# Kernel tuning notes

Hardware: AMD Instinct MI355X
Metric: run time of the kernel (lower is better)

Reference implementation:

```python
import jax, jax.numpy as jnp
import numpy as np
import math

N_HEADS = 16
HEAD_DIM = 128  # dim=2048 / 16


def _rope(t, cos, sin):
    # t: [B, S, H, hd]; cos/sin: [1, S, hd//2]
    B, S, H, hd = t.shape
    tr = t.reshape(B, S, H, hd // 2, 2)
    te, to = tr[..., 0], tr[..., 1]
    c = cos[:, :, None, :]
    s = sin[:, :, None, :]
    oe = te * c - to * s
    oo = te * s + to * c
    return jnp.stack([oe, oo], axis=-1).reshape(B, S, H, hd)


def setup_inputs() -> dict:
    key = jax.random.key(0)
    ks = jax.random.split(key, 5)
    B, S, D = 2, 2048, 2048
    hd = HEAD_DIM
    scale = 1.0 / math.sqrt(D)
    x = jax.random.normal(ks[0], (B, S, D), dtype=jnp.float32)
    wq = jax.random.normal(ks[1], (D, D), dtype=jnp.float32) * scale
    wk = jax.random.normal(ks[2], (D, D), dtype=jnp.float32) * scale
    wv = jax.random.normal(ks[3], (D, D), dtype=jnp.float32) * scale
    wo = jax.random.normal(ks[4], (D, D), dtype=jnp.float32) * scale
    # true RoPE angles: freqs = base^(-2i/hd), angles = pos * freqs
    base = 10000.0
    inv_freq = 1.0 / (base ** (np.arange(0, hd, 2, dtype=np.float32) / hd))  # [hd//2]
    pos = np.arange(S, dtype=np.float32)
    ang = pos[:, None] * inv_freq[None, :]  # [S, hd//2]
    pos_cos = jnp.asarray(np.cos(ang))[None]  # [1, S, hd//2]
    pos_sin = jnp.asarray(np.sin(ang))[None]
    return {"x": x, "wq": wq, "wk": wk, "wv": wv, "wo": wo,
            "pos_cos": pos_cos, "pos_sin": pos_sin}


def reference(x, wq, wk, wv, wo, pos_cos, pos_sin):
    B, S, D = x.shape
    H, hd = N_HEADS, HEAD_DIM
    # nn.Linear: y = x @ W.T
    q = (x @ wq.T).reshape(B, S, H, hd)
    k = (x @ wk.T).reshape(B, S, H, hd)
    v = (x @ wv.T).reshape(B, S, H, hd)
    q = _rope(q, pos_cos, pos_sin)
    k = _rope(k, pos_cos, pos_sin)
    # naive full attention, softmax in fp32 (as original)
    scores = jnp.einsum('bqhd,bkhd->bhqk', q, k) / math.sqrt(hd)
    probs = jax.nn.softmax(scores.astype(jnp.float32), axis=-1).astype(q.dtype)
    out = jnp.einsum('bhqk,bkhd->bqhd', probs, v).reshape(B, S, H * hd)
    return out @ wo.T
```

## Files before the change

### kernel.cpp

```cpp
#include <hip/hip_runtime.h>
#include <hip/hip_bf16.h>

typedef __attribute__((ext_vector_type(8))) short short8;
typedef __attribute__((ext_vector_type(4))) float f32x4;
typedef __attribute__((ext_vector_type(16))) float f32x16;
typedef __attribute__((ext_vector_type(8))) unsigned short ushort8v;
typedef __attribute__((ext_vector_type(4))) unsigned int u32x4;

#define AS_GLOBAL __attribute__((address_space(1)))
#define AS_LDS    __attribute__((address_space(3)))

__device__ __forceinline__ void async_ld16(const void* src, void* lds) {
  __builtin_amdgcn_global_load_lds((const AS_GLOBAL unsigned int*)src,
                                   (AS_LDS unsigned int*)lds, 16, 0, 0);
}

__device__ __forceinline__ unsigned short f2bf(float f) {
  unsigned int u = __float_as_uint(f);
  u = (u + 0x7fffu + ((u >> 16) & 1u)) >> 16;
  return (unsigned short)u;
}

__global__ void cvt_bf16(const float* __restrict__ x,  const float* __restrict__ wq,
                         const float* __restrict__ wk, const float* __restrict__ wvv,
                         const float* __restrict__ wo,
                         unsigned short* __restrict__ xb,  unsigned short* __restrict__ wqb,
                         unsigned short* __restrict__ wkb, unsigned short* __restrict__ wvb,
                         unsigned short* __restrict__ wob)
{
  const int NX = 8388608, NW = 4194304;
  const int total = (NX + 4 * NW) >> 3;
  for (int v = blockIdx.x * blockDim.x + threadIdx.x; v < total;
       v += gridDim.x * blockDim.x) {
    int base = v << 3;
    const float* src; unsigned short* dst; int off;
    if (base < NX) { src = x; dst = xb; off = base; }
    else {
      int t = base - NX; int w = t >> 22; off = t & (NW - 1);
      src = (w == 0) ? wq : (w == 1) ? wk : (w == 2) ? wvv : wo;
      dst = (w == 0) ? wqb : (w == 1) ? wkb : (w == 2) ? wvb : wob;
    }
    float4 f0 = *(const float4*)(src + off);
    float4 f1 = *(const float4*)(src + off + 4);
    ushort8v o;
    o[0] = f2bf(f0.x); o[1] = f2bf(f0.y); o[2] = f2bf(f0.z); o[3] = f2bf(f0.w);
    o[4] = f2bf(f1.x); o[5] = f2bf(f1.y); o[6] = f2bf(f1.z); o[7] = f2bf(f1.w);
    *(ushort8v*)(dst + off) = o;
  }
}

#define BM 128
#define BN 128
#define BKT 64

template<int MODE>
__global__ __launch_bounds__(256, 3) void gemm_bt(
    const short* __restrict__ A, const short* __restrict__ B,
    void* __restrict__ C, int M, int N, int K,
    const float* __restrict__ pcos, const float* __restrict__ psin)
{
  __shared__ short As[BM * BKT];
  __shared__ short Bs[BN * BKT];

  const int tid  = threadIdx.x;
  const int lane = tid & 63;
  const int wv   = tid >> 6;
  const int wr   = (wv >> 1) << 6;
  const int wc   = (wv & 1) << 6;
  const int l15  = lane & 15;
  const int lg   = lane >> 4;

  const int nbn = N >> 7;
  const int nwg = gridDim.x;
  int id = blockIdx.x;
  id = (id & 7) * (nwg >> 3) + (id >> 3);
  const int m0 = (id / nbn) << 7;
  const int n0 = (id % nbn) << 7;

  f32x4 acc[4][4] = {};

  for (int kt = 0; kt < K; kt += BKT) {
    __syncthreads();
#pragma unroll
    for (int i = 0; i < 4; ++i) {
      int c = i * 256 + tid;
      int r = c >> 3;
      int colb = (c & 7) << 4;
      int scol = colb ^ ((r & 7) << 4);
      async_ld16((const char*)A + (((size_t)(m0 + r) * K + kt) << 1) + scol,
                 (char*)As + c * 16);
    }
#pragma unroll
    for (int i = 0; i < 4; ++i) {
      int c = i * 256 + tid;
      int r = c >> 3;
      int colb = (c & 7) << 4;
      int scol = colb ^ ((r & 7) << 4);
      async_ld16((const char*)B + (((size_t)(n0 + r) * K + kt) << 1) + scol,
                 (char*)Bs + c * 16);
    }
    __syncthreads();

#pragma unroll
    for (int kk = 0; kk < 2; ++kk) {
      const int kb = (kk << 6) + (lg << 4);
      short8 af[4], bf[4];
#pragma unroll
      for (int mi = 0; mi < 4; ++mi) {
        int row = wr + (mi << 4) + l15;
        af[mi] = *(const short8*)((const char*)As + (row << 7) + (kb ^ ((row & 7) << 4)));
      }
#pragma unroll
      for (int ni = 0; ni < 4; ++ni) {
        int row = wc + (ni << 4) + l15;
        bf[ni] = *(const short8*)((const char*)Bs + (row << 7) + (kb ^ ((row & 7) << 4)));
      }
#pragma unroll
      for (int mi = 0; mi < 4; ++mi)
#pragma unroll
        for (int ni = 0; ni < 4; ++ni)
          acc[mi][ni] = __builtin_amdgcn_mfma_f32_16x16x32_bf16(
              af[mi], bf[ni], acc[mi][ni], 0, 0, 0);
    }
  }

#pragma unroll
  for (int mi = 0; mi < 4; ++mi) {
#pragma unroll
    for (int ni = 0; ni < 4; ++ni) {
      const int col  = n0 + wc + (ni << 4) + l15;
      const int row0 = m0 + wr + (mi << 4) + (lg << 2);
      if (MODE == 0) {
#pragma unroll
        for (int r = 0; r < 4; ++r)
          ((unsigned short*)C)[(size_t)(row0 + r) * N + col] = f2bf(acc[mi][ni][r]);
      } else if (MODE == 1) {
        const int d = col & 127;
        const int j = d >> 1;
#pragma unroll
        for (int r = 0; r < 4; ++r) {
          int s = (row0 + r) & 2047;
          float cv = pcos[(s << 6) + j];
          float sv = psin[(s << 6) + j];
          float v  = acc[mi][ni][r];
          float pv = __shfl_xor(v, 1, 64);
          float o  = (d & 1) ? (pv * sv + v * cv) : (v * cv - pv * sv);
          ((unsigned short*)C)[(size_t)(row0 + r) * N + col] = f2bf(o);
        }
      } else if (MODE == 2) {
        const int h = col >> 7, d = col & 127;
        const int b = row0 >> 11, s = row0 & 2047;
        unsigned long long pk =
              (unsigned long long)f2bf(acc[mi][ni][0])
            | ((unsigned long long)f2bf(acc[mi][ni][1]) << 16)
            | ((unsigned long long)f2bf(acc[mi][ni][2]) << 32)
            | ((unsigned long long)f2bf(acc[mi][ni][3]) << 48);
        *(unsigned long long*)((unsigned short*)C +
            (((((size_t)b << 4) + h) << 7) + d) * 2048 + s) = pk;
      } else {
#pragma unroll
        for (int r = 0; r < 4; ++r)
          ((float*)C)[(size_t)(row0 + r) * N + col] = acc[mi][ni][r];
      }
    }
  }
}

__global__ __launch_bounds__(512, 2) void flash_fwd2(
    const short* __restrict__ Q, const short* __restrict__ Kg,
    const short* __restrict__ VT, unsigned short* __restrict__ O)
{
  __shared__ short Ks[2][64 * 128];
  __shared__ short Vs[2][128 * 64];

  const int tid = threadIdx.x;
  const int lane = tid & 63;
  const int w   = tid >> 6;
  const int l31 = lane & 31;
  const int hi  = lane >> 5;

  const int bh   = blockIdx.y;
  const int b    = bh >> 4;
  const int q0   = blockIdx.x << 8;
  const int hcol = (bh & 15) << 7;

  short8 qf[8];
  {
    const short* qp = Q + (((size_t)((b << 11) + q0 + (w << 5) + l31)) << 11)
                        + hcol + (hi << 3);
#pragma unroll
    for (int dk = 0; dk < 8; ++dk)
      qf[dk] = *(const short8*)(qp + (dk << 4));
  }

  const char* kS0 = (const char*)Kg +
      (((((size_t)(b << 11)) + (tid >> 4)) << 11) + hcol) * 2 +
      (((tid & 15) << 4) ^ (((tid >> 4) & 15) << 4));
  const char* kS1 = (const char*)Kg +
      (((((size_t)(b << 11)) + 32 + (tid >> 4)) << 11) + hcol) * 2 +
      (((tid & 15) << 4) ^ (((tid >> 4) & 15) << 4));
  const char* vS0 = (const char*)VT +
      (((size_t)((bh << 7) + (tid >> 3))) << 12) +
      (((tid & 7) << 4) ^ (((tid >> 3) & 7) << 4));
  const char* vS1 = vS0 + ((size_t)64 << 12);

#define STAGE(t, bf) do {                                              \
    size_t ko = (size_t)(t) * 262144; int vo = (t) * 128;              \
    async_ld16(kS0 + ko, (char*)Ks[bf] + tid * 16);                    \
    async_ld16(kS1 + ko, (char*)Ks[bf] + (tid + 512) * 16);            \
    async_ld16(vS0 + vo, (char*)Vs[bf] + tid * 16);                    \
    async_ld16(vS1 + vo, (char*)Vs[bf] + (tid + 512) * 16);            \
  } while (0)

  f32x16 oacc[4] = {};
  float M = -3e38f, l = 0.f;
  const float cl2 = 0.1275313940154099f;

  STAGE(0, 0);
  int cur = 0;

  const int kxor = (l31 & 15) << 4;

  for (int t = 0; t < 32; ++t) {
    __builtin_amdgcn_s_barrier();
    asm volatile("" ::: "memory");
    if (t < 31) {
      STAGE(t + 1, cur ^ 1);
      asm volatile("s_waitcnt vmcnt(4)" ::: "memory");
    } else {
      asm volatile("s_waitcnt vmcnt(0)" ::: "memory");
    }
    __builtin_amdgcn_s_barrier();
    asm volatile("" ::: "memory");

    const char* kb = (const char*)Ks[cur];
    const char* vb = (const char*)Vs[cur];

    f32x16 s0 = {}, s1 = {};
#pragma unroll
    for (int dk = 0; dk < 8; ++dk) {
      const int cb = ((dk << 5) + (hi << 4)) ^ kxor;
      short8 kf0 = *(const short8*)(kb + (l31 << 8) + cb);
      short8 kf1 = *(const short8*)(kb + ((32 + l31) << 8) + cb);
      s0 = __builtin_amdgcn_mfma_f32_32x32x16_bf16(kf0, qf[dk], s0, 0, 0, 0);
      s1 = __builtin_amdgcn_mfma_f32_32x32x16_bf16(kf1, qf[dk], s1, 0, 0, 0);
    }

    float tmax = s0[0];
#pragma unroll
    for (int r = 1; r < 16; ++r) tmax = fmaxf(tmax, s0[r]);
#pragma unroll
    for (int r = 0; r < 16; ++r) tmax = fmaxf(tmax, s1[r]);
    tmax = fmaxf(tmax, __shfl_xor(tmax, 32, 64));
    tmax *= cl2;
    if (!__all(tmax <= M + 8.f)) {
      float mnew = fmaxf(M, tmax);
      float alpha = __builtin_amdgcn_exp2f(M - mnew);
      M = mnew;
      l *= alpha;
#pragma unroll
      for (int nd = 0; nd < 4; ++nd) oacc[nd] = oacc[nd] * alpha;
    }
    float psum = 0.f;
#pragma unroll
    for (int r = 0; r < 16; ++r) {
      float p = __builtin_amdgcn_exp2f(s0[r] * cl2 - M);
      s0[r] = p; psum += p;
    }
#pragma unroll
    for (int r = 0; r < 16; ++r) {
      float p = __builtin_amdgcn_exp2f(s1[r] * cl2 - M);
      s1[r] = p; psum += p;
    }
    psum += __shfl_xor(psum, 32, 64);
    l += psum;

#pragma unroll
    for (int ks = 0; ks < 4; ++ks) {
      const int base = (ks & 1) << 3;
      float p0, p1, p2, p3, p4, p5, p6, p7;
      if (ks < 2) {
        p0 = s0[base + 0]; p1 = s0[base + 1]; p2 = s0[base + 2]; p3 = s0[base + 3];
        p4 = s0[base + 4]; p5 = s0[base + 5]; p6 = s0[base + 6]; p7 = s0[base + 7];
      } else {
        p0 = s1[base + 0]; p1 = s1[base + 1]; p2 = s1[base + 2]; p3 = s1[base + 3];
        p4 = s1[base + 4]; p5 = s1[base + 5]; p6 = s1[base + 6]; p7 = s1[base + 7];
      }
      unsigned int X, Y, Z, W;
      asm("v_cvt_pk_bf16_f32 %0, %1, %2" : "=v"(X) : "v"(p0), "v"(p1));
      asm("v_cvt_pk_bf16_f32 %0, %1, %2" : "=v"(Y) : "v"(p2), "v"(p3));
      asm("v_cvt_pk_bf16_f32 %0, %1, %2" : "=v"(Z) : "v"(p4), "v"(p5));
      asm("v_cvt_pk_bf16_f32 %0, %1, %2" : "=v"(W) : "v"(p6), "v"(p7));
      unsigned int SX = (unsigned int)__shfl_xor((int)X, 32, 64);
      unsigned int SY = (unsigned int)__shfl_xor((int)Y, 32, 64);
      unsigned int SZ = (unsigned int)__shfl_xor((int)Z, 32, 64);
      unsigned int SW = (unsigned int)__shfl_xor((int)W, 32, 64);
      u32x4 pw;
      pw[0] = hi ? SZ : X;
      pw[1] = hi ? SW : Y;
      pw[2] = hi ? Z  : SX;
      pw[3] = hi ? W  : SY;
      short8 pa = __builtin_bit_cast(short8, pw);
#pragma unroll
      for (int nd = 0; nd < 4; ++nd) {
        const int row = (nd << 5) + l31;
        short8 vf = *(const short8*)(vb + (row << 7) +
                     (((ks << 5) + (hi << 4)) ^ ((row & 7) << 4)));
        oacc[nd] = __builtin_amdgcn_mfma_f32_32x32x16_bf16(pa, vf, oacc[nd], 0, 0, 0);
      }
    }
    cur ^= 1;
  }
#undef STAGE

  const float linv = 1.f / l;
  float lr[16];
#pragma unroll
  for (int r = 0; r < 16; ++r)
    lr[r] = __shfl(linv, (r & 3) + ((r >> 2) << 3) + (hi << 2), 64);

  const size_t orow0 = (size_t)((b << 11) + q0 + (w << 5));
#pragma unroll
  for (int nd = 0; nd < 4; ++nd) {
#pragma unroll
    for (int r = 0; r < 16; ++r) {
      const int crow = (r & 3) + ((r >> 2) << 3) + (hi << 2);
      O[((orow0 + crow) << 11) + hcol + (nd << 5) + l31] =
          f2bf(oacc[nd][r] * lr[r]);
    }
  }
}

extern "C" void kernel_launch(void* const* d_in, const int* in_sizes, int n_in,
                              void* d_out, int out_size, void* d_ws, size_t ws_size,
                              hipStream_t stream)
{
  (void)in_sizes; (void)n_in; (void)out_size; (void)ws_size;
  const float* x    = (const float*)d_in[0];
  const float* wq   = (const float*)d_in[1];
  const float* wk   = (const float*)d_in[2];
  const float* wv   = (const float*)d_in[3];
  const float* wo   = (const float*)d_in[4];
  const float* pcos = (const float*)d_in[5];
  const float* psin = (const float*)d_in[6];

  char* ws = (char*)d_ws;
  short* xb  = (short*)(ws);
  short* wqb = (short*)(ws + 16777216);
  short* wkb = (short*)(ws + 25165824);
  short* wvb = (short*)(ws + 33554432);
  short* wob = (short*)(ws + 41943040);
  short* Qr  = (short*)(ws + 50331648);
  short* Kr  = (short*)(ws + 67108864);
  short* VT  = (short*)(ws + 83886080);
  short* At  = xb;

  cvt_bf16<<<2048, 256, 0, stream>>>(x, wq, wk, wv, wo,
      (unsigned short*)xb, (unsigned short*)wqb, (unsigned short*)wkb,
      (unsigned short*)wvb, (unsigned short*)wob);

  gemm_bt<1><<<512, 256, 0, stream>>>(xb, wqb, Qr, 4096, 2048, 2048, pcos, psin);
  gemm_bt<1><<<512, 256, 0, stream>>>(xb, wkb, Kr, 4096, 2048, 2048, pcos, psin);
  gemm_bt<2><<<512, 256, 0, stream>>>(xb, wvb, VT, 4096, 2048, 2048, nullptr, nullptr);

  flash_fwd2<<<dim3(8, 32), 512, 0, stream>>>(Qr, Kr, VT, (unsigned short*)At);

  gemm_bt<3><<<512, 256, 0, stream>>>(At, wob, d_out, 4096, 2048, 2048, nullptr, nullptr);
}
```

Baseline: 379.5 us.

## Fuse QKV projections into one 256x128 double-buffered GEMM with split B staging

Replaces the three separate Q/K/V projection GEMMs with one launch over a concatenated N=6144 weight (wq, wk, wv are contiguous in the workspace). The epilogue routes columns to either the RoPE'd Q/K output or the transposed V layout. The GEMM moves to 512-thread blocks with 256x128 tiles and double-buffered LDS, prefetching the next A tile while the current B halves are consumed, with s_setprio around the MFMA bursts. This cuts launch count and synchronization stalls, but uses more LDS per block and leaves fewer blocks for the output projection.

Result: no change. 378.4 us (-0.3%).

```diff
diff --git a/kernel.cpp b/kernel.cpp
--- a/kernel.cpp
+++ b/kernel.cpp
@@ -49,24 +49,20 @@
   }
 }
 
-#define BM 128
-#define BN 128
-#define BKT 64
-
 template<int MODE>
-__global__ __launch_bounds__(256, 3) void gemm_bt(
+__global__ __launch_bounds__(512, 2) void gemm8(
     const short* __restrict__ A, const short* __restrict__ B,
-    void* __restrict__ C, int M, int N, int K,
+    unsigned short* __restrict__ Cqk, unsigned short* __restrict__ Cvt,
+    float* __restrict__ Cf, int M, int N, int K,
     const float* __restrict__ pcos, const float* __restrict__ psin)
 {
-  __shared__ short As[BM * BKT];
-  __shared__ short Bs[BN * BKT];
+  __shared__ short L[2][24576];
 
   const int tid  = threadIdx.x;
   const int lane = tid & 63;
-  const int wv   = tid >> 6;
-  const int wr   = (wv >> 1) << 6;
-  const int wc   = (wv & 1) << 6;
+  const int w    = tid >> 6;
+  const int wm   = w >> 1;
+  const int wn   = w & 1;
   const int l15  = lane & 15;
   const int lg   = lane >> 4;
 
@@ -74,69 +70,127 @@
   const int nwg = gridDim.x;
   int id = blockIdx.x;
   id = (id & 7) * (nwg >> 3) + (id >> 3);
-  const int m0 = (id / nbn) << 7;
+  const int m0 = (id / nbn) << 8;
   const int n0 = (id % nbn) << 7;
 
+  const char* aS[4];
+  const char* bS[2];
+#pragma unroll
+  for (int i = 0; i < 4; ++i) {
+    int c = i * 512 + tid;
+    int r = c >> 3;
+    int scol = ((c & 7) << 4) ^ ((r & 7) << 4);
+    aS[i] = (const char*)A + (((size_t)(m0 + r) * K) << 1) + scol;
+  }
+#pragma unroll
+  for (int i = 0; i < 2; ++i) {
+    int c = i * 512 + tid;
+    int r = c >> 3;
+    int scol = ((c & 7) << 4) ^ ((r & 7) << 4);
+    bS[i] = (const char*)B + (((size_t)(n0 + r) * K) << 1) + scol;
+  }
+
+#define STAGE_A(t, buf) do {                                            \
+    const size_t ko_ = (size_t)(t) << 7;                                \
+    _Pragma("unroll")                                                   \
+    for (int i_ = 0; i_ < 4; ++i_)                                      \
+      async_ld16(aS[i_] + ko_, (char*)L[buf] + (i_ * 512 + tid) * 16);  \
+  } while (0)
+#define STAGE_B(t, buf) do {                                            \
+    const size_t ko_ = (size_t)(t) << 7;                                \
+    _Pragma("unroll")                                                   \
+    for (int i_ = 0; i_ < 2; ++i_)                                      \
+      async_ld16(bS[i_] + ko_,                                          \
+                 (char*)L[buf] + 32768 + (i_ * 512 + tid) * 16);        \
+  } while (0)
+
   f32x4 acc[4][4] = {};
-
-  for (int kt = 0; kt < K; kt += BKT) {
-    __syncthreads();
-#pragma unroll
-    for (int i = 0; i < 4; ++i) {
-      int c = i * 256 + tid;
-      int r = c >> 3;
-      int colb = (c & 7) << 4;
-      int scol = colb ^ ((r & 7) << 4);
-      async_ld16((const char*)A + (((size_t)(m0 + r) * K + kt) << 1) + scol,
-                 (char*)As + c * 16);
-    }
-#pragma unroll
-    for (int i = 0; i < 4; ++i) {
-      int c = i * 256 + tid;
-      int r = c >> 3;
-      int colb = (c & 7) << 4;
-      int scol = colb ^ ((r & 7) << 4);
-      async_ld16((const char*)B + (((size_t)(n0 + r) * K + kt) << 1) + scol,
-                 (char*)Bs + c * 16);
-    }
-    __syncthreads();
-
-#pragma unroll
-    for (int kk = 0; kk < 2; ++kk) {
-      const int kb = (kk << 6) + (lg << 4);
-      short8 af[4], bf[4];
-#pragma unroll
-      for (int mi = 0; mi < 4; ++mi) {
-        int row = wr + (mi << 4) + l15;
-        af[mi] = *(const short8*)((const char*)As + (row << 7) + (kb ^ ((row & 7) << 4)));
+  const int T = K >> 6;
+
+  STAGE_A(0, 0);
+  STAGE_B(0, 0);
+
+  for (int t = 0; t < T; ++t) {
+    const int rb = t & 1, sb = rb ^ 1;
+    const char* Lr = (const char*)L[rb];
+
+    if (t + 1 < T) {
+      STAGE_A(t + 1, sb);
+      asm volatile("s_waitcnt vmcnt(4)" ::: "memory");
+    } else {
+      asm volatile("s_waitcnt vmcnt(0)" ::: "memory");
+    }
+    __builtin_amdgcn_s_barrier();
+    asm volatile("" ::: "memory");
+
+    short8 af[4][2], bf[2][2];
+#pragma unroll
+    for (int mi = 0; mi < 4; ++mi) {
+      const int ra = (wm << 6) + (mi << 4) + l15;
+      const int sx = (ra & 7) << 4;
+      af[mi][0] = *(const short8*)(Lr + (ra << 7) + ((lg << 4) ^ sx));
+      af[mi][1] = *(const short8*)(Lr + (ra << 7) + ((64 + (lg << 4)) ^ sx));
+    }
+#pragma unroll
+    for (int nj = 0; nj < 2; ++nj) {
+      const int rn = (wn << 6) + (nj << 4) + l15;
+      const int sx = (rn & 7) << 4;
+      bf[nj][0] = *(const short8*)(Lr + 32768 + (rn << 7) + ((lg << 4) ^ sx));
+      bf[nj][1] = *(const short8*)(Lr + 32768 + (rn << 7) + ((64 + (lg << 4)) ^ sx));
+    }
+    __builtin_amdgcn_s_setprio(1);
+#pragma unroll
+    for (int mi = 0; mi < 4; ++mi)
+#pragma unroll
+      for (int nj = 0; nj < 2; ++nj) {
+        acc[mi][nj] = __builtin_amdgcn_mfma_f32_16x16x32_bf16(
+            af[mi][0], bf[nj][0], acc[mi][nj], 0, 0, 0);
+        acc[mi][nj] = __builtin_amdgcn_mfma_f32_16x16x32_bf16(
+            af[mi][1], bf[nj][1], acc[mi][nj], 0, 0, 0);
       }
-#pragma unroll
-      for (int ni = 0; ni < 4; ++ni) {
-        int row = wc + (ni << 4) + l15;
-        bf[ni] = *(const short8*)((const char*)Bs + (row << 7) + (kb ^ ((row & 7) << 4)));
+    __builtin_amdgcn_s_setprio(0);
+    __builtin_amdgcn_s_barrier();
+    asm volatile("" ::: "memory");
+
+    if (t + 1 < T) STAGE_B(t + 1, sb);
+#pragma unroll
+    for (int nj = 0; nj < 2; ++nj) {
+      const int rn = (wn << 6) + ((nj + 2) << 4) + l15;
+      const int sx = (rn & 7) << 4;
+      bf[nj][0] = *(const short8*)(Lr + 32768 + (rn << 7) + ((lg << 4) ^ sx));
+      bf[nj][1] = *(const short8*)(Lr + 32768 + (rn << 7) + ((64 + (lg << 4)) ^ sx));
+    }
+    __builtin_amdgcn_s_setprio(1);
+#pragma unroll
+    for (int mi = 0; mi < 4; ++mi)
+#pragma unroll
+      for (int nj = 0; nj < 2; ++nj) {
+        acc[mi][nj + 2] = __builtin_amdgcn_mfma_f32_16x16x32_bf16(
+            af[mi][0], bf[nj][0], acc[mi][nj + 2], 0, 0, 0);
+        acc[mi][nj + 2] = __builtin_amdgcn_mfma_f32_16x16x32_bf16(
+            af[mi][1], bf[nj][1], acc[mi][nj + 2], 0, 0, 0);
       }
-#pragma unroll
-      for (int mi = 0; mi < 4; ++mi)
-#pragma unroll
-        for (int ni = 0; ni < 4; ++ni)
-          acc[mi][ni] = __builtin_amdgcn_mfma_f32_16x16x32_bf16(
-              af[mi], bf[ni], acc[mi][ni], 0, 0, 0);
-    }
-  }
+    __builtin_amdgcn_s_setprio(0);
+    __builtin_amdgcn_s_barrier();
+    asm volatile("" ::: "memory");
+  }
+#undef STAGE_A
+#undef STAGE_B
 
 #pragma unroll
   for (int mi = 0; mi < 4; ++mi) {
 #pragma unroll
     for (int ni = 0; ni < 4; ++ni) {
-      const int col  = n0 + wc + (ni << 4) + l15;
-      const int row0 = m0 + wr + (mi << 4) + (lg << 2);
-      if (MODE == 0) {
+      const int col  = n0 + (wn << 6) + (ni << 4) + l15;
+      const int row0 = m0 + (wm << 6) + (mi << 4) + (lg << 2);
+      if (MODE == 1) {
 #pragma unroll
         for (int r = 0; r < 4; ++r)
-          ((unsigned short*)C)[(size_t)(row0 + r) * N + col] = f2bf(acc[mi][ni][r]);
-      } else if (MODE == 1) {
+          Cf[(size_t)(row0 + r) * N + col] = acc[mi][ni][r];
+      } else if (col < 4096) {
         const int d = col & 127;
         const int j = d >> 1;
+        unsigned short* dst = Cqk + ((size_t)(col >> 11) << 23);
 #pragma unroll
         for (int r = 0; r < 4; ++r) {
           int s = (row0 + r) & 2047;
@@ -145,22 +199,19 @@
           float v  = acc[mi][ni][r];
           float pv = __shfl_xor(v, 1, 64);
           float o  = (d & 1) ? (pv * sv + v * cv) : (v * cv - pv * sv);
-          ((unsigned short*)C)[(size_t)(row0 + r) * N + col] = f2bf(o);
+          dst[((size_t)(row0 + r) << 11) + (col & 2047)] = f2bf(o);
         }
-      } else if (MODE == 2) {
-        const int h = col >> 7, d = col & 127;
+      } else {
+        const int vc = col & 2047;
+        const int h = vc >> 7, d = vc & 127;
         const int b = row0 >> 11, s = row0 & 2047;
         unsigned long long pk =
               (unsigned long long)f2bf(acc[mi][ni][0])
             | ((unsigned long long)f2bf(acc[mi][ni][1]) << 16)
             | ((unsigned long long)f2bf(acc[mi][ni][2]) << 32)
             | ((unsigned long long)f2bf(acc[mi][ni][3]) << 48);
-        *(unsigned long long*)((unsigned short*)C +
+        *(unsigned long long*)(Cvt +
             (((((size_t)b << 4) + h) << 7) + d) * 2048 + s) = pk;
-      } else {
-#pragma unroll
-        for (int r = 0; r < 4; ++r)
-          ((float*)C)[(size_t)(row0 + r) * N + col] = acc[mi][ni][r];
       }
     }
   }
@@ -359,11 +410,13 @@
       (unsigned short*)xb, (unsigned short*)wqb, (unsigned short*)wkb,
       (unsigned short*)wvb, (unsigned short*)wob);
 
-  gemm_bt<1><<<512, 256, 0, stream>>>(xb, wqb, Qr, 4096, 2048, 2048, pcos, psin);
-  gemm_bt<1><<<512, 256, 0, stream>>>(xb, wkb, Kr, 4096, 2048, 2048, pcos, psin);
-  gemm_bt<2><<<512, 256, 0, stream>>>(xb, wvb, VT, 4096, 2048, 2048, nullptr, nullptr);
+  gemm8<0><<<768, 512, 0, stream>>>(xb, wqb,
+      (unsigned short*)Qr, (unsigned short*)VT, nullptr,
+      4096, 6144, 2048, pcos, psin);
 
   flash_fwd2<<<dim3(8, 32), 512, 0, stream>>>(Qr, Kr, VT, (unsigned short*)At);
 
-  gemm_bt<3><<<512, 256, 0, stream>>>(At, wob, d_out, 4096, 2048, 2048, nullptr, nullptr);
-}
+  gemm8<1><<<256, 512, 0, stream>>>(At, wob,
+      nullptr, nullptr, (float*)d_out,
+      4096, 2048, 2048, nullptr, nullptr);
+}
```
